# Optimization experiments

Measured on AMD Instinct MI355X. Metric: run time of the kernel, lower is better.

## Reference

```python
import jax, jax.numpy as jnp
import numpy as np

E, U, D, R = 200000, 50000, 128, 32
N2, N1, NU = 100000, 80000, 20000  # hop-2 frontier, hop-1 frontier, unreachable; N1+N2+NU == E
M1, M0 = 1600000, 800000


def setup_inputs() -> dict:
    key = jax.random.key(0)
    ks = jax.random.split(key, 16)
    inp = {
        'ent_emb': jax.random.normal(ks[0], (E, D), jnp.float32) * 0.1,
        'user_emb': jax.random.normal(ks[1], (U, D), jnp.float32) * 0.1,
        'rel_emb': jax.random.normal(ks[2], (R, D), jnp.float32) * 0.1,
        'W_self': jax.random.normal(ks[3], (D, D), jnp.float32) / np.sqrt(D),
        'W_nei': jax.random.normal(ks[4], (D, D), jnp.float32) / np.sqrt(D),
        'b': jnp.zeros((D,), jnp.float32),
        'final_indices': jax.random.randint(ks[5], (N2,), 0, E, jnp.int32),
        'ent_now1': jax.random.randint(ks[6], (N1,), 0, E, jnp.int32),
        'e1_src': jax.random.randint(ks[7], (M1,), 0, N2, jnp.int32),
        'e1_dst': jax.random.randint(ks[8], (M1,), 0, N1, jnp.int32),
        'e1_rel': jax.random.randint(ks[9], (M1,), 0, R, jnp.int32),
        'e0_src': jax.random.randint(ks[10], (M0,), 0, N1, jnp.int32),
        'e0_dst': jax.random.randint(ks[11], (M0,), 0, U, jnp.int32),
        'e0_rel': jax.random.randint(ks[12], (M0,), 0, R, jnp.int32),
        'unreach_idx': jax.random.randint(ks[13], (NU,), 0, E, jnp.int32),
        'order': jax.random.permutation(ks[14], E).astype(jnp.int32),
    }
    return inp


def _rgcn_layer(x, tail, src, dst, rel, W_self, W_nei, b, rel_emb, n_out, activate):
    # self transform: [N, D]
    out = x @ W_self + b
    if tail is not None:
        # gather neighbor reps + relation modulation: [M, D]
        msg = tail[src] * rel_emb[rel]
        agg = jax.ops.segment_sum(msg, dst, num_segments=n_out)
        deg = jax.ops.segment_sum(jnp.ones_like(dst, dtype=x.dtype), dst, num_segments=n_out)
        agg = agg / jnp.clip(deg, 1.0)[:, None]
        out = out + agg @ W_nei
    return jnp.tanh(out) if activate else out


def reference(ent_emb, user_emb, rel_emb, W_self, W_nei, b,
              final_indices, ent_now1, e1_src, e1_dst, e1_rel,
              e0_src, e0_dst, e0_rel, unreach_idx, order):
    # hop 2: raw gathered entity embeddings (deepest frontier)
    h2 = ent_emb[final_indices]                                            # [N2, D]
    # hop 1: RGCN over kg edges from hop-2 frontier
    h1 = _rgcn_layer(ent_emb[ent_now1], h2, e1_src, e1_dst, e1_rel,
                     W_self, W_nei, b, rel_emb, N1, activate=True)          # [N1, D]
    # hop 0: user representations, no activation (activate=False in source)
    user_rep = _rgcn_layer(user_emb, h1, e0_src, e0_dst, e0_rel,
                           W_self, W_nei, b, rel_emb, U, activate=False)    # [U, D]
    # unreachable entities: self-only transform (tail_rep=None)
    unreachable = _rgcn_layer(ent_emb[unreach_idx], None, None, None, None,
                              W_self, W_nei, b, rel_emb, NU, activate=True)  # [NU, D]
    # concat hop reps in forward hop order, then reindex-scatter by entity order
    ent_user_all = jnp.concatenate([h1, h2, unreachable], axis=0)[order]    # [E, D]
    return jnp.concatenate([user_rep, ent_user_all], axis=0)               # [U+E, D]
```

## Files before the change

kernel.cpp:

```cpp
#include <hip/hip_runtime.h>

#define E_  200000
#define U_  50000
#define D_  128
#define R_  32
#define N2_ 100000
#define N1_ 80000
#define NU_ 20000
#define M1_ 1600000
#define M0_ 800000

__device__ __forceinline__ float4 ld4(const float* p) {
    return *reinterpret_cast<const float4*>(p);
}
__device__ __forceinline__ void st4(float* p, float4 v) {
    *reinterpret_cast<float4*>(p) = v;
}

__device__ __forceinline__ float fast_tanh(float x) {
    float e = __expf(2.0f * x);
    return 1.0f - 2.0f / (e + 1.0f);
}

__global__ __launch_bounds__(256) void gather_rows_k(
    const float* __restrict__ src, const int* __restrict__ idx,
    float* __restrict__ out, int n)
{
    long long gid = (long long)blockIdx.x * blockDim.x + threadIdx.x;
    int i = (int)(gid >> 5);
    int l = (int)(gid & 31);
    if (i >= n) return;
    int s = idx[i];
    st4(out + (long long)i * 128 + l * 4, ld4(src + (long long)s * 128 + l * 4));
}

__global__ __launch_bounds__(256) void hist_k(
    const int* __restrict__ dst, int* __restrict__ cnt, int M)
{
    int i = blockIdx.x * blockDim.x + threadIdx.x;
    if (i < M) atomicAdd(&cnt[dst[i]], 1);
}

__global__ __launch_bounds__(256) void partial_sums_k(
    const int* __restrict__ cnt, int* __restrict__ bsum, int N)
{
    __shared__ int sm[256];
    const int t = threadIdx.x;
    const int base = blockIdx.x * 1024;
    int sum = 0;
    #pragma unroll
    for (int i = 0; i < 4; ++i) {
        int g = base + t + i * 256;
        if (g < N) sum += cnt[g];
    }
    sm[t] = sum;
    __syncthreads();
    #pragma unroll
    for (int s = 128; s > 0; s >>= 1) {
        if (t < s) sm[t] += sm[t + s];
        __syncthreads();
    }
    if (t == 0) bsum[blockIdx.x] = sm[0];
}

__global__ __launch_bounds__(256) void scan_partials_k(
    int* __restrict__ bsum, int NB, int* __restrict__ off, int N)
{
    __shared__ int ls[256];
    const int t = threadIdx.x;
    int v = (t < NB) ? bsum[t] : 0;
    ls[t] = v;
    __syncthreads();
    #pragma unroll
    for (int d = 1; d < 256; d <<= 1) {
        int u = (t >= d) ? ls[t - d] : 0;
        __syncthreads();
        ls[t] += u;
        __syncthreads();
    }
    if (t < NB) bsum[t] = ls[t] - v;
    if (t == 255) off[N] = ls[255];
}

__global__ __launch_bounds__(256) void scan_apply_k(
    const int* __restrict__ cnt, const int* __restrict__ bsum,
    int* __restrict__ off, int* __restrict__ cur, int N)
{
    __shared__ int buf[1024];
    __shared__ int ts[256];
    const int t = threadIdx.x;
    const int base = blockIdx.x * 1024;
    #pragma unroll
    for (int i = 0; i < 4; ++i) {
        int g = base + t + i * 256;
        buf[t + i * 256] = (g < N) ? cnt[g] : 0;
    }
    __syncthreads();
    const int a = buf[t * 4], b = buf[t * 4 + 1], c = buf[t * 4 + 2], d = buf[t * 4 + 3];
    const int s = a + b + c + d;
    ts[t] = s;
    __syncthreads();
    #pragma unroll
    for (int dd = 1; dd < 256; dd <<= 1) {
        int u = (t >= dd) ? ts[t - dd] : 0;
        __syncthreads();
        ts[t] += u;
        __syncthreads();
    }
    const int pre = bsum[blockIdx.x] + ts[t] - s;
    const int o0 = pre, o1 = pre + a, o2 = o1 + b, o3 = o2 + c;
    const int g0 = base + t * 4;
    if (g0 + 3 < N) {
        *reinterpret_cast<int4*>(off + g0) = make_int4(o0, o1, o2, o3);
        *reinterpret_cast<int4*>(cur + g0) = make_int4(o0, o1, o2, o3);
    } else {
        if (g0     < N) { off[g0]     = o0; cur[g0]     = o0; }
        if (g0 + 1 < N) { off[g0 + 1] = o1; cur[g0 + 1] = o1; }
        if (g0 + 2 < N) { off[g0 + 2] = o2; cur[g0 + 2] = o2; }
    }
}

__global__ __launch_bounds__(256) void fill_k(
    const int* __restrict__ src, const int* __restrict__ dst,
    const int* __restrict__ rel, int* __restrict__ cur,
    int* __restrict__ sorted, int M)
{
    int i = blockIdx.x * blockDim.x + threadIdx.x;
    if (i >= M) return;
    int p = atomicAdd(&cur[dst[i]], 1);
    sorted[p] = src[i] | (rel[i] << 20);
}

__global__ __launch_bounds__(256) void seg_reduce_k(
    const float* __restrict__ tail, const float* __restrict__ rel_emb,
    const int* __restrict__ off, const int* __restrict__ sorted,
    float* __restrict__ aggout, int N)
{
    long long gid = (long long)blockIdx.x * blockDim.x + threadIdx.x;
    int row = (int)(gid >> 5);
    int l = (int)(gid & 31) * 4;
    if (row >= N) return;
    int s = off[row], e = off[row + 1];
    float4 acc = make_float4(0.f, 0.f, 0.f, 0.f);
    int j = s;
    for (; j + 1 < e; j += 2) {
        int p0 = sorted[j], p1 = sorted[j + 1];
        float4 t0 = ld4(tail + (long long)(p0 & 0xFFFFF) * 128 + l);
        float4 r0 = ld4(rel_emb + (long long)(p0 >> 20) * 128 + l);
        float4 t1 = ld4(tail + (long long)(p1 & 0xFFFFF) * 128 + l);
        float4 r1 = ld4(rel_emb + (long long)(p1 >> 20) * 128 + l);
        acc.x = fmaf(t0.x, r0.x, acc.x); acc.y = fmaf(t0.y, r0.y, acc.y);
        acc.z = fmaf(t0.z, r0.z, acc.z); acc.w = fmaf(t0.w, r0.w, acc.w);
        acc.x = fmaf(t1.x, r1.x, acc.x); acc.y = fmaf(t1.y, r1.y, acc.y);
        acc.z = fmaf(t1.z, r1.z, acc.z); acc.w = fmaf(t1.w, r1.w, acc.w);
    }
    if (j < e) {
        int p0 = sorted[j];
        float4 t0 = ld4(tail + (long long)(p0 & 0xFFFFF) * 128 + l);
        float4 r0 = ld4(rel_emb + (long long)(p0 >> 20) * 128 + l);
        acc.x = fmaf(t0.x, r0.x, acc.x); acc.y = fmaf(t0.y, r0.y, acc.y);
        acc.z = fmaf(t0.z, r0.z, acc.z); acc.w = fmaf(t0.w, r0.w, acc.w);
    }
    float sc = 1.0f / (float)max(e - s, 1);
    acc.x *= sc; acc.y *= sc; acc.z *= sc; acc.w *= sc;
    st4(aggout + (long long)row * 128 + l, acc);
}

template<bool GATHER, bool ACCUM, bool BIAS, bool ACT>
__global__ __launch_bounds__(256) void gemm_rows_k(
    const float* __restrict__ X, const int* __restrict__ idx,
    const float* __restrict__ W, const float* __restrict__ bias,
    float* __restrict__ Out, int N)
{
    __shared__ float XsT[32][128];
    __shared__ float Ws [32][128];
    const int tid = threadIdx.x;
    const int rowbase = blockIdx.x * 128;
    const int r0 = (tid >> 4) * 8;
    const int c0 = (tid & 15) * 8;

    float acc[8][8];
    if (BIAS) {
        #pragma unroll
        for (int j = 0; j < 8; ++j) {
            float bv = bias[c0 + j];
            #pragma unroll
            for (int i = 0; i < 8; ++i) acc[i][j] = bv;
        }
    } else {
        #pragma unroll
        for (int i = 0; i < 8; ++i)
            #pragma unroll
            for (int j = 0; j < 8; ++j) acc[i][j] = 0.0f;
    }

    const int srow = tid >> 3;
    const int skq  = (tid & 7) * 4;
    const int sswz = (tid & 7) << 2;
    const int wkk  = tid >> 5;
    const int wcc  = (tid & 31) * 4;

    for (int k0 = 0; k0 < 128; k0 += 32) {
        __syncthreads();
        #pragma unroll
        for (int p = 0; p < 4; ++p) {
            int row = p * 32 + srow;
            int grow = rowbase + row;
            int cl = grow < N ? grow : (N - 1);
            const float* xr = GATHER ? X + (long long)idx[cl] * 128
                                     : X + (long long)cl * 128;
            float4 v = ld4(xr + k0 + skq);
            int rs = row ^ sswz;
            XsT[skq + 0][rs] = v.x;
            XsT[skq + 1][rs] = v.y;
            XsT[skq + 2][rs] = v.z;
            XsT[skq + 3][rs] = v.w;
        }
        #pragma unroll
        for (int p = 0; p < 4; ++p) {
            int k = p * 8 + wkk;
            st4(&Ws[k][wcc], ld4(W + (long long)(k0 + k) * 128 + wcc));
        }
        __syncthreads();
        #pragma unroll
        for (int k = 0; k < 32; ++k) {
            int A0 = (((r0 >> 2) ^ ((k >> 2) & 7)) << 2);
            float4 x0 = ld4(&XsT[k][A0]);
            float4 x1 = ld4(&XsT[k][A0 ^ 4]);
            float4 w0 = ld4(&Ws[k][c0]);
            float4 w1 = ld4(&Ws[k][c0 + 4]);
            float xs[8] = {x0.x, x0.y, x0.z, x0.w, x1.x, x1.y, x1.z, x1.w};
            float ws[8] = {w0.x, w0.y, w0.z, w0.w, w1.x, w1.y, w1.z, w1.w};
            #pragma unroll
            for (int i = 0; i < 8; ++i)
                #pragma unroll
                for (int j = 0; j < 8; ++j)
                    acc[i][j] = fmaf(xs[i], ws[j], acc[i][j]);
        }
    }

    #pragma unroll
    for (int i = 0; i < 8; ++i) {
        int row = rowbase + r0 + i;
        if (row >= N) continue;
        float* op = Out + (long long)row * 128 + c0;
        float vals[8];
        #pragma unroll
        for (int j = 0; j < 8; ++j) vals[j] = acc[i][j];
        if (ACCUM) {
            float4 o0 = ld4(op), o1 = ld4(op + 4);
            vals[0] += o0.x; vals[1] += o0.y; vals[2] += o0.z; vals[3] += o0.w;
            vals[4] += o1.x; vals[5] += o1.y; vals[6] += o1.z; vals[7] += o1.w;
        }
        if (ACT) {
            #pragma unroll
            for (int j = 0; j < 8; ++j) vals[j] = fast_tanh(vals[j]);
        }
        st4(op,     make_float4(vals[0], vals[1], vals[2], vals[3]));
        st4(op + 4, make_float4(vals[4], vals[5], vals[6], vals[7]));
    }
}

template<bool GATHER1, bool ACT>
__global__ __launch_bounds__(256) void gemm_fused_k(
    const float* __restrict__ X1, const int* __restrict__ idx,
    const float* __restrict__ X2,
    const float* __restrict__ W1, const float* __restrict__ W2,
    const float* __restrict__ bias, float* __restrict__ Out, int N)
{
    __shared__ float X1sT[32][128];
    __shared__ float X2sT[32][128];
    __shared__ float W1s [32][128];
    __shared__ float W2s [32][128];
    const int tid = threadIdx.x;
    const int rowbase = blockIdx.x * 128;
    const int r0 = (tid >> 4) * 8;
    const int c0 = (tid & 15) * 8;

    float acc[8][8];
    #pragma unroll
    for (int j = 0; j < 8; ++j) {
        float bv = bias[c0 + j];
        #pragma unroll
        for (int i = 0; i < 8; ++i) acc[i][j] = bv;
    }

    const int srow = tid >> 3;
    const int skq  = (tid & 7) * 4;
    const int sswz = (tid & 7) << 2;
    const int wkk  = tid >> 5;
    const int wcc  = (tid & 31) * 4;

    for (int k0 = 0; k0 < 128; k0 += 32) {
        __syncthreads();
        #pragma unroll
        for (int p = 0; p < 4; ++p) {
            int row = p * 32 + srow;
            int grow = rowbase + row;
            int cl = grow < N ? grow : (N - 1);
            const float* x1r = GATHER1 ? X1 + (long long)idx[cl] * 128
                                       : X1 + (long long)cl * 128;
            const float* x2r = X2 + (long long)cl * 128;
            float4 v1 = ld4(x1r + k0 + skq);
            float4 v2 = ld4(x2r + k0 + skq);
            int rs = row ^ sswz;
            X1sT[skq + 0][rs] = v1.x; X1sT[skq + 1][rs] = v1.y;
            X1sT[skq + 2][rs] = v1.z; X1sT[skq + 3][rs] = v1.w;
            X2sT[skq + 0][rs] = v2.x; X2sT[skq + 1][rs] = v2.y;
            X2sT[skq + 2][rs] = v2.z; X2sT[skq + 3][rs] = v2.w;
        }
        #pragma unroll
        for (int p = 0; p < 4; ++p) {
            int k = p * 8 + wkk;
            st4(&W1s[k][wcc], ld4(W1 + (long long)(k0 + k) * 128 + wcc));
            st4(&W2s[k][wcc], ld4(W2 + (long long)(k0 + k) * 128 + wcc));
        }
        __syncthreads();
        #pragma unroll
        for (int k = 0; k < 32; ++k) {
            int A0 = (((r0 >> 2) ^ ((k >> 2) & 7)) << 2);
            float4 a0 = ld4(&X1sT[k][A0]);
            float4 a1 = ld4(&X1sT[k][A0 ^ 4]);
            float4 b0 = ld4(&X2sT[k][A0]);
            float4 b1 = ld4(&X2sT[k][A0 ^ 4]);
            float4 u0 = ld4(&W1s[k][c0]);
            float4 u1 = ld4(&W1s[k][c0 + 4]);
            float4 v0 = ld4(&W2s[k][c0]);
            float4 v1 = ld4(&W2s[k][c0 + 4]);
            float x1s[8] = {a0.x, a0.y, a0.z, a0.w, a1.x, a1.y, a1.z, a1.w};
            float x2s[8] = {b0.x, b0.y, b0.z, b0.w, b1.x, b1.y, b1.z, b1.w};
            float w1s[8] = {u0.x, u0.y, u0.z, u0.w, u1.x, u1.y, u1.z, u1.w};
            float w2s[8] = {v0.x, v0.y, v0.z, v0.w, v1.x, v1.y, v1.z, v1.w};
            #pragma unroll
            for (int i = 0; i < 8; ++i)
                #pragma unroll
                for (int j = 0; j < 8; ++j) {
                    acc[i][j] = fmaf(x1s[i], w1s[j], acc[i][j]);
                    acc[i][j] = fmaf(x2s[i], w2s[j], acc[i][j]);
                }
        }
    }

    #pragma unroll
    for (int i = 0; i < 8; ++i) {
        int row = rowbase + r0 + i;
        if (row >= N) continue;
        float* op = Out + (long long)row * 128 + c0;
        float vals[8];
        #pragma unroll
        for (int j = 0; j < 8; ++j) vals[j] = acc[i][j];
        if (ACT) {
            #pragma unroll
            for (int j = 0; j < 8; ++j) vals[j] = fast_tanh(vals[j]);
        }
        st4(op,     make_float4(vals[0], vals[1], vals[2], vals[3]));
        st4(op + 4, make_float4(vals[4], vals[5], vals[6], vals[7]));
    }
}

extern "C" void kernel_launch(void* const* d_in, const int* in_sizes, int n_in,
                              void* d_out, int out_size, void* d_ws, size_t ws_size,
                              hipStream_t stream)
{
    const float* ent_emb  = (const float*)d_in[0];
    const float* user_emb = (const float*)d_in[1];
    const float* rel_emb  = (const float*)d_in[2];
    const float* W_self   = (const float*)d_in[3];
    const float* W_nei    = (const float*)d_in[4];
    const float* bvec     = (const float*)d_in[5];
    const int* final_indices = (const int*)d_in[6];
    const int* ent_now1   = (const int*)d_in[7];
    const int* e1_src     = (const int*)d_in[8];
    const int* e1_dst     = (const int*)d_in[9];
    const int* e1_rel     = (const int*)d_in[10];
    const int* e0_src     = (const int*)d_in[11];
    const int* e0_dst     = (const int*)d_in[12];
    const int* e0_rel     = (const int*)d_in[13];
    const int* unreach_idx = (const int*)d_in[14];
    const int* order      = (const int*)d_in[15];

    float* out = (float*)d_out;
    float* ws  = (float*)d_ws;

    float* concat = ws;
    float* agg1 = concat + (size_t)E_ * 128;
    float* agg0 = agg1 + (size_t)N1_ * 128;
    int* cur1 = (int*)(agg0 + (size_t)U_ * 128);
    int* cur0 = cur1 + N1_;
    int* off1 = cur0 + U_;
    int* off0 = off1 + (N1_ + 4);
    int* bsum1 = off0 + (U_ + 4);
    int* bsum0 = bsum1 + 256;
    int* sorted1 = bsum0 + 256;
    int* sorted0 = sorted1 + M1_;

    float* h1   = concat;
    float* h2   = concat + (size_t)N1_ * 128;
    float* unre = concat + (size_t)(N1_ + N2_) * 128;

    const int NB1 = (N1_ + 1023) / 1024;
    const int NB0 = (U_  + 1023) / 1024;

    hipMemsetAsync(cur1, 0, (size_t)(N1_ + U_) * sizeof(int), stream);

    gather_rows_k<<<(N2_ * 32 + 255) / 256, 256, 0, stream>>>(
        ent_emb, final_indices, h2, N2_);

    hist_k<<<(M1_ + 255) / 256, 256, 0, stream>>>(e1_dst, cur1, M1_);
    partial_sums_k<<<NB1, 256, 0, stream>>>(cur1, bsum1, N1_);
    scan_partials_k<<<1, 256, 0, stream>>>(bsum1, NB1, off1, N1_);
    scan_apply_k<<<NB1, 256, 0, stream>>>(cur1, bsum1, off1, cur1, N1_);
    fill_k<<<(M1_ + 255) / 256, 256, 0, stream>>>(
        e1_src, e1_dst, e1_rel, cur1, sorted1, M1_);
    seg_reduce_k<<<(N1_ * 32 + 255) / 256, 256, 0, stream>>>(
        h2, rel_emb, off1, sorted1, agg1, N1_);

    gemm_fused_k<true, true><<<(N1_ + 127) / 128, 256, 0, stream>>>(
        ent_emb, ent_now1, agg1, W_self, W_nei, bvec, h1, N1_);

    hist_k<<<(M0_ + 255) / 256, 256, 0, stream>>>(e0_dst, cur0, M0_);
    partial_sums_k<<<NB0, 256, 0, stream>>>(cur0, bsum0, U_);
    scan_partials_k<<<1, 256, 0, stream>>>(bsum0, NB0, off0, U_);
    scan_apply_k<<<NB0, 256, 0, stream>>>(cur0, bsum0, off0, cur0, U_);
    fill_k<<<(M0_ + 255) / 256, 256, 0, stream>>>(
        e0_src, e0_dst, e0_rel, cur0, sorted0, M0_);
    seg_reduce_k<<<(U_ * 32 + 255) / 256, 256, 0, stream>>>(
        h1, rel_emb, off0, sorted0, agg0, U_);

    gemm_fused_k<false, false><<<(U_ + 127) / 128, 256, 0, stream>>>(
        user_emb, nullptr, agg0, W_self, W_nei, bvec, out, U_);

    gemm_rows_k<true, false, true, true><<<(NU_ + 127) / 128, 256, 0, stream>>>(
        ent_emb, unreach_idx, W_self, bvec, unre, NU_);

    gather_rows_k<<<(E_ * 32 + 255) / 256, 256, 0, stream>>>(
        concat, order, out + (size_t)U_ * 128, E_);
}
```

Measured before the change: 912.2 us.

## Replace random-scatter CSR fill with two-pass bucketed binning by destination

Measured after the change: 931.9 us. 2.2% more time.

```diff
diff --git a/kernel.cpp b/kernel.cpp
--- a/kernel.cpp
+++ b/kernel.cpp
@@ -9,6 +9,9 @@
 #define NU_ 20000
 #define M1_ 1600000
 #define M0_ 800000
+
+#define NBUCK1 313
+#define NBUCK0 196
 
 __device__ __forceinline__ float4 ld4(const float* p) {
     return *reinterpret_cast<const float4*>(p);
@@ -120,15 +123,67 @@
     }
 }
 
-__global__ __launch_bounds__(256) void fill_k(
+__global__ __launch_bounds__(256) void init_bcur_k(
+    const int* __restrict__ off, int* __restrict__ bcur, int nbuck)
+{
+    int i = blockIdx.x * blockDim.x + threadIdx.x;
+    if (i < nbuck) bcur[i] = off[i << 8];
+}
+
+#define EPB 2048
+__global__ __launch_bounds__(256) void bin_k(
     const int* __restrict__ src, const int* __restrict__ dst,
-    const int* __restrict__ rel, int* __restrict__ cur,
-    int* __restrict__ sorted, int M)
-{
-    int i = blockIdx.x * blockDim.x + threadIdx.x;
-    if (i >= M) return;
-    int p = atomicAdd(&cur[dst[i]], 1);
-    sorted[p] = src[i] | (rel[i] << 20);
+    const int* __restrict__ rel, int* __restrict__ bcur,
+    int* __restrict__ bdst, int* __restrict__ bsr, int M, int nbuck)
+{
+    __shared__ int hist[384];
+    __shared__ int base[384];
+    const int t = threadIdx.x;
+    const int e0 = blockIdx.x * EPB;
+    for (int i = t; i < nbuck; i += 256) hist[i] = 0;
+    __syncthreads();
+    int dv[8], sv[8], rv[8];
+    #pragma unroll
+    for (int i = 0; i < 8; ++i) {
+        int e = e0 + i * 256 + t;
+        if (e < M) {
+            dv[i] = dst[e]; sv[i] = src[e]; rv[i] = rel[e];
+            atomicAdd(&hist[dv[i] >> 8], 1);
+        } else dv[i] = -1;
+    }
+    __syncthreads();
+    for (int i = t; i < nbuck; i += 256) {
+        int c = hist[i];
+        base[i] = c ? atomicAdd(&bcur[i], c) : 0;
+        hist[i] = 0;
+    }
+    __syncthreads();
+    #pragma unroll
+    for (int i = 0; i < 8; ++i) {
+        if (dv[i] >= 0) {
+            int bk = dv[i] >> 8;
+            int p = base[bk] + atomicAdd(&hist[bk], 1);
+            bdst[p] = dv[i];
+            bsr[p] = sv[i] | (rv[i] << 20);
+        }
+    }
+}
+
+__global__ __launch_bounds__(256) void fill2_k(
+    const int* __restrict__ bdst, const int* __restrict__ bsr,
+    const int* __restrict__ off, int* __restrict__ cur,
+    int* __restrict__ sorted, int N)
+{
+    int b = blockIdx.x;
+    int rs = off[b << 8];
+    int reidx = (b + 1) << 8;
+    if (reidx > N) reidx = N;
+    int re = off[reidx];
+    for (int j = rs + threadIdx.x; j < re; j += 256) {
+        int d = bdst[j];
+        int p = atomicAdd(&cur[d], 1);
+        sorted[p] = bsr[j];
+    }
 }
 
 __global__ __launch_bounds__(256) void seg_reduce_k(
@@ -391,8 +446,13 @@
     int* off0 = off1 + (N1_ + 4);
     int* bsum1 = off0 + (U_ + 4);
     int* bsum0 = bsum1 + 256;
-    int* sorted1 = bsum0 + 256;
+    int* bcur1 = bsum0 + 256;
+    int* bcur0 = bcur1 + 320;
+    int* sorted1 = bcur0 + 320;
     int* sorted0 = sorted1 + M1_;
+
+    int* bdst = (int*)agg1;
+    int* bsr  = bdst + M1_;
 
     float* h1   = concat;
     float* h2   = concat + (size_t)N1_ * 128;
@@ -410,8 +470,10 @@
     partial_sums_k<<<NB1, 256, 0, stream>>>(cur1, bsum1, N1_);
     scan_partials_k<<<1, 256, 0, stream>>>(bsum1, NB1, off1, N1_);
     scan_apply_k<<<NB1, 256, 0, stream>>>(cur1, bsum1, off1, cur1, N1_);
-    fill_k<<<(M1_ + 255) / 256, 256, 0, stream>>>(
-        e1_src, e1_dst, e1_rel, cur1, sorted1, M1_);
+    init_bcur_k<<<2, 256, 0, stream>>>(off1, bcur1, NBUCK1);
+    bin_k<<<(M1_ + EPB - 1) / EPB, 256, 0, stream>>>(
+        e1_src, e1_dst, e1_rel, bcur1, bdst, bsr, M1_, NBUCK1);
+    fill2_k<<<NBUCK1, 256, 0, stream>>>(bdst, bsr, off1, cur1, sorted1, N1_);
     seg_reduce_k<<<(N1_ * 32 + 255) / 256, 256, 0, stream>>>(
         h2, rel_emb, off1, sorted1, agg1, N1_);
 
@@ -422,8 +484,10 @@
     partial_sums_k<<<NB0, 256, 0, stream>>>(cur0, bsum0, U_);
     scan_partials_k<<<1, 256, 0, stream>>>(bsum0, NB0, off0, U_);
     scan_apply_k<<<NB0, 256, 0, stream>>>(cur0, bsum0, off0, cur0, U_);
-    fill_k<<<(M0_ + 255) / 256, 256, 0, stream>>>(
-        e0_src, e0_dst, e0_rel, cur0, sorted0, M0_);
+    init_bcur_k<<<1, 256, 0, stream>>>(off0, bcur0, NBUCK0);
+    bin_k<<<(M0_ + EPB - 1) / EPB, 256, 0, stream>>>(
+        e0_src, e0_dst, e0_rel, bcur0, bdst, bsr, M0_, NBUCK0);
+    fill2_k<<<NBUCK0, 256, 0, stream>>>(bdst, bsr, off0, cur0, sorted0, U_);
     seg_reduce_k<<<(U_ * 32 + 255) / 256, 256, 0, stream>>>(
         h1, rel_emb, off0, sorted0, agg0, U_);
 
```
